# Optimization experiments

Hardware: AMD Instinct MI355X
Metric: run time of the kernel (lower is better)

The kernel has to match this reference:

```python
import jax, jax.numpy as jnp
import numpy as np

B, C, N, K, H = 8, 32, 4096, 32, 4  # batch, d_model, num_points, knn, heads
D = C // H
LN_EPS = 1e-5
ATT_EPS = 1e-6


def setup_inputs() -> dict:
    key = jax.random.key(0)
    ks = jax.random.split(key, 12)
    s = 0.05
    return {
        "search_feat": jax.random.normal(ks[0], (B, C, N), jnp.float32),
        "search_xyz": jax.random.normal(ks[1], (B, N, 3), jnp.float32),
        # pos MLP: Linear(3,32)+ReLU+Linear(32,32), weights stored [in,out]
        "w_pos1": jax.random.normal(ks[2], (3, 32), jnp.float32) * s,
        "b_pos1": jnp.zeros((32,), jnp.float32),
        "w_pos2": jax.random.normal(ks[3], (32, 32), jnp.float32) * s,
        "b_pos2": jnp.zeros((32,), jnp.float32),
        "w_q": jax.random.normal(ks[4], (C, C), jnp.float32) * s,
        "w_k": jax.random.normal(ks[5], (C, C), jnp.float32) * s,
        "w_v": jax.random.normal(ks[6], (C, C), jnp.float32) * s,
        "w_merge": jax.random.normal(ks[7], (C, C), jnp.float32) * s,
        "ln1_g": jnp.ones((C,), jnp.float32),
        "ln1_b": jnp.zeros((C,), jnp.float32),
        "w_mlp1": jax.random.normal(ks[8], (2 * C, 2 * C), jnp.float32) * s,
        "w_mlp2": jax.random.normal(ks[9], (2 * C, C), jnp.float32) * s,
        "ln2_g": jnp.ones((C,), jnp.float32),
        "ln2_b": jnp.zeros((C,), jnp.float32),
    }


def _layernorm(x, g, b):
    m = jnp.mean(x, axis=-1, keepdims=True)
    v = jnp.mean((x - m) ** 2, axis=-1, keepdims=True)
    return g * (x - m) * jax.lax.rsqrt(v + LN_EPS) + b


def _elu1(x):
    return jax.nn.elu(x) + 1.0


def reference(search_feat, search_xyz, w_pos1, b_pos1, w_pos2, b_pos2,
              w_q, w_k, w_v, w_merge, ln1_g, ln1_b, w_mlp1, w_mlp2,
              ln2_g, ln2_b):
    b, c, n = search_feat.shape
    h, d, k = H, C // H, K

    xt = jnp.transpose(search_feat, (0, 2, 1))  # [B,N,C]
    # knn in feature space: pd = -||xi||^2 + 2 xi.xj - ||xj||^2 (neg sq dist)
    xx = jnp.sum(xt * xt, axis=-1)  # [B,N]
    pd = 2.0 * jnp.einsum('bnc,bmc->bnm', xt, xt) - xx[:, :, None] - xx[:, None, :]
    idx = jax.lax.top_k(pd, k)[1]  # [B,N,K] nearest (incl. self)

    gather = jax.vmap(lambda f, i: f[i])  # per-batch gather
    fea_knn = gather(xt, idx)            # [B,N,K,C]
    xyz_knn = gather(search_xyz, idx)    # [B,N,K,3]

    def pos_mlp(z):
        return jax.nn.relu(z @ w_pos1 + b_pos1) @ w_pos2 + b_pos2

    q_in = xt + pos_mlp(search_xyz)      # [B,N,C]  (query, L=1)
    kv_in = fea_knn + pos_mlp(xyz_knn)   # [B,N,K,C]

    Q = (q_in @ w_q).reshape(b, n, h, d)          # [B,N,H,D]
    Ky = (kv_in @ w_k).reshape(b, n, k, h, d)     # [B,N,K,H,D]
    V = (kv_in @ w_v).reshape(b, n, k, h, d)

    Qf = _elu1(Q)
    Kf = _elu1(Ky)
    Vn = V / k  # v_length = K
    KV = jnp.einsum('bnkhd,bnkhv->bnhdv', Kf, Vn)
    Z = 1.0 / (jnp.einsum('bnhd,bnhd->bnh', Qf, Kf.sum(axis=2)) + ATT_EPS)
    msg = jnp.einsum('bnhd,bnhdv,bnh->bnhv', Qf, KV, Z) * k  # [B,N,H,D]

    msg = msg.reshape(b, n, c) @ w_merge
    msg = _layernorm(msg, ln1_g, ln1_b)
    msg = jnp.concatenate([xt, msg], axis=-1)          # [B,N,2C]
    msg = jax.nn.relu(msg @ w_mlp1) @ w_mlp2           # [B,N,C]
    msg = _layernorm(msg, ln2_g, ln2_b)
    return jnp.transpose(xt + msg, (0, 2, 1))          # [B,C,N]
```

## Files before the change

kernel.cpp:

```cpp
#include <hip/hip_runtime.h>
#include <math.h>

#define BB 8
#define CC 32
#define NN 4096
#define KNN 32
#define NP (BB*NN)

#define OFF_XT  0u
#define OFF_QF  1048576u
#define OFF_KV  2097152u
#define OFF_XX  4194304u
#define OFF_IDX 4227072u
#define OFF_XH  5275648u
#define OFF_XL  5799936u
#define OFF_MSG 5275648u

typedef _Float16 f16x8 __attribute__((ext_vector_type(8)));
typedef float f32x4 __attribute__((ext_vector_type(4)));
typedef float f32x16 __attribute__((ext_vector_type(16)));
#define MFMA16(A,B,C) __builtin_amdgcn_mfma_f32_16x16x32_f16(A,B,C,0,0,0)
#define MFMA32(A,B,C) __builtin_amdgcn_mfma_f32_32x32x16_f16(A,B,C,0,0,0)

__device__ __forceinline__ float elu1(float x) {
    return x > 0.f ? x + 1.f : expf(x);
}

__global__ __launch_bounds__(256) void k_transpose(const float* __restrict__ feat,
                                                   float* __restrict__ xt,
                                                   _Float16* __restrict__ Xh,
                                                   _Float16* __restrict__ Xl,
                                                   float* __restrict__ xx) {
    __shared__ float tile[32][65];
    int b = blockIdx.y;
    int n0 = blockIdx.x * 64;
    int t = threadIdx.x;
    int nn = t & 63, cr = t >> 6;
#pragma unroll
    for (int r = 0; r < 8; ++r) {
        int c = r * 4 + cr;
        tile[c][nn] = feat[((size_t)b * 32 + c) * NN + n0 + nn];
    }
    __syncthreads();
    int c2 = t & 31, nr = t >> 5;
#pragma unroll
    for (int r = 0; r < 8; ++r) {
        int nl = r * 8 + nr;
        size_t gi = ((size_t)b * NN + n0 + nl) * 32 + c2;
        float v = tile[c2][nl];
        xt[gi] = v;
        _Float16 hv = (_Float16)v;
        Xh[gi] = hv;
        Xl[gi] = (_Float16)(v - (float)hv);
    }
    if (t < 64) {
        float s = 0.f;
#pragma unroll
        for (int c = 0; c < 32; ++c) { float u = tile[c][t]; s += u * u; }
        xx[(size_t)b * NN + n0 + t] = s;
    }
}

__global__ __launch_bounds__(256, 2) void k_prep(
        const float* __restrict__ xt, const float* __restrict__ xyz,
        const float* __restrict__ w_pos1, const float* __restrict__ b_pos1,
        const float* __restrict__ w_pos2, const float* __restrict__ b_pos2,
        const float* __restrict__ w_q, const float* __restrict__ w_k,
        const float* __restrict__ w_v,
        float* __restrict__ Qf, float* __restrict__ KV) {
    __shared__ float sW2[1024], sWq[1024], sWk[1024], sWv[1024];
    int t = threadIdx.x;
    for (int i = t; i < 1024; i += 256) {
        sW2[i] = w_pos2[i];
        sWq[i] = w_q[i];
        sWk[i] = w_k[i];
        sWv[i] = w_v[i];
    }
    int lane = t & 31;
    int g = t >> 5;
    float w1c0 = w_pos1[lane], w1c1 = w_pos1[32 + lane], w1c2 = w_pos1[64 + lane];
    float b1c = b_pos1[lane], b2c = b_pos2[lane];
    __syncthreads();
#pragma unroll 1
    for (int p = blockIdx.x * 8 + g; p < NP; p += gridDim.x * 8) {
        asm volatile("" ::: "memory");
        float x0 = xyz[(size_t)p * 3 + 0];
        float x1 = xyz[(size_t)p * 3 + 1];
        float x2 = xyz[(size_t)p * 3 + 2];
        float h = fmaxf(x0 * w1c0 + x1 * w1c1 + x2 * w1c2 + b1c, 0.f);
        float P = b2c;
#pragma unroll 8
        for (int j = 0; j < 32; ++j) P += __shfl(h, j, 32) * sW2[j * 32 + lane];
        float xv = xt[(size_t)p * 32 + lane];
        float qin = xv + P;
        float qa = 0.f, ka = 0.f, va = 0.f;
#pragma unroll 8
        for (int j = 0; j < 32; ++j) {
            float qj = __shfl(qin, j, 32);
            qa += qj * sWq[j * 32 + lane];
            ka += qj * sWk[j * 32 + lane];
            va += qj * sWv[j * 32 + lane];
        }
        Qf[(size_t)p * 32 + lane] = elu1(qa);
        float2 kvv;
        kvv.x = elu1(ka);
        kvv.y = va;
        *(((float2*)(KV + (size_t)p * 64)) + lane) = kvv;
    }
}

__global__ __launch_bounds__(256, 2) void k_knn(
        const _Float16* __restrict__ Xh, const _Float16* __restrict__ Xl,
        const float* __restrict__ xt, const float* __restrict__ xx,
        unsigned* __restrict__ idxg) {
    __shared__ unsigned histU[32 * 132];
    __shared__ unsigned outIdx[32][32];
    __shared__ unsigned tieIdx[32][128];
    __shared__ int sT[32];
    __shared__ unsigned sBase[32];
    __shared__ unsigned outCnt[32], tieCnt[32];
    __shared__ float sM2;
    __shared__ float redbuf[4];

    int bid = blockIdx.x;
    int b = bid & 7;
    int n0 = (bid >> 3) << 5;
    int t = threadIdx.x;
    int lane = t & 63, wv = t >> 6;
    size_t bbase = (size_t)b * NN;

    for (int i = t; i < 32 * 132; i += 256) histU[i] = 0u;
    if (t < 32) { outCnt[t] = 0u; tieCnt[t] = 0u; }

    float lm = 0.f;
    for (int i = t; i < NN; i += 256) lm = fmaxf(lm, xx[bbase + i]);
#pragma unroll
    for (int off = 32; off >= 1; off >>= 1) lm = fmaxf(lm, __shfl_xor(lm, off, 64));
    if (lane == 0) redbuf[wv] = lm;
    __syncthreads();
    if (t == 0) sM2 = fmaxf(fmaxf(redbuf[0], redbuf[1]), fmaxf(redbuf[2], redbuf[3]));
    __syncthreads();
    float M = fmaxf(sM2, 1e-20f);

    const float C127 = 127.99f;
    float s = C127 / (4.f * M);
    float s2 = s + s;
    float sneg = -s;
    float o = 3.f * s * M;

    int cl31 = lane & 31;
    int hi = lane >> 5;
    int hi4 = hi << 2;
    const _Float16* Xhb = Xh + bbase * 32;
    const _Float16* Xlb = Xl + bbase * 32;
    const float* xxb = xx + bbase;

    const _Float16* ArH = Xhb + (size_t)(n0 + cl31) * 32;
    const _Float16* ArL = Xlb + (size_t)(n0 + cl31) * 32;
    f16x8 AhA = *(const f16x8*)(ArH + hi * 8);
    f16x8 AhB = *(const f16x8*)(ArH + 16 + hi * 8);
    f16x8 AlA = *(const f16x8*)(ArL + hi * 8);
    f16x8 AlB = *(const f16x8*)(ArL + 16 + hi * 8);

    unsigned colbase = (unsigned)(wv * 1024);
    unsigned hiB = (unsigned)hi * 16u;
    const char* XhbB = (const char*)Xhb;
    const char* XlbB = (const char*)Xlb;
    unsigned hi528 = (unsigned)hi * 528u;

    {
        unsigned cpc = colbase + cl31;
        f16x8 BhA_c = *(const f16x8*)(XhbB + cpc * 64u + hiB);
        f16x8 BhB_c = *(const f16x8*)(XhbB + cpc * 64u + hiB + 32u);
        f16x8 BlA_c = *(const f16x8*)(XlbB + cpc * 64u + hiB);
        f16x8 BlB_c = *(const f16x8*)(XlbB + cpc * 64u + hiB + 32u);
        float xxj_c = xxb[cpc];
#pragma unroll 1
        for (int tt = 0; tt < 32; ++tt) {
            unsigned cpn = colbase + (unsigned)(((tt + 1) & 31) << 5) + cl31;
            f16x8 BhA_n = *(const f16x8*)(XhbB + cpn * 64u + hiB);
            f16x8 BhB_n = *(const f16x8*)(XhbB + cpn * 64u + hiB + 32u);
            f16x8 BlA_n = *(const f16x8*)(XlbB + cpn * 64u + hiB);
            f16x8 BlB_n = *(const f16x8*)(XlbB + cpn * 64u + hiB + 32u);
            float xxj_n = xxb[cpn];
            f32x16 acc = {0.f};
            acc = MFMA32(AhA, BlA_c, acc); acc = MFMA32(AhB, BlB_c, acc);
            acc = MFMA32(AlA, BhA_c, acc); acc = MFMA32(AlB, BhB_c, acc);
            acc = MFMA32(AhA, BhA_c, acc); acc = MFMA32(AhB, BhB_c, acc);
            float e = __builtin_fmaf(sneg, xxj_c, o);
#pragma unroll
            for (int r = 0; r < 16; ++r) {
                float qv = __builtin_fmaf(acc[r], s2, e);
                float qc = fminf(qv, C127);
                unsigned bkt = (unsigned)qc;
                atomicAdd(&histU[(unsigned)(((r & 3) + 8 * (r >> 2)) * 132) + hi528 + bkt], 1u);
            }
            BhA_c = BhA_n; BhB_c = BhB_n; BlA_c = BlA_n; BlB_c = BlB_n; xxj_c = xxj_n;
        }
    }
    __syncthreads();

#pragma unroll 1
    for (int rr = 0; rr < 8; ++rr) {
        int row = wv * 8 + rr;
        const unsigned* Hr = histU + row * 132;
        unsigned cl = Hr[2 * lane], ch = Hr[2 * lane + 1];
        unsigned ss = cl + ch;
        unsigned acc = ss;
#pragma unroll
        for (int off = 1; off < 64; off <<= 1) {
            unsigned vv = __shfl_down(acc, off, 64);
            if (lane + off < 64) acc += vv;
        }
        unsigned run = acc - ss;
        int Tl = -1; unsigned bl = 0;
        if (run < 32u && run + ch >= 32u) { Tl = 2 * lane + 1; bl = run; }
        run += ch;
        if (Tl < 0 && run < 32u && run + cl >= 32u) { Tl = 2 * lane; bl = run; }
        unsigned long long bal = __ballot(Tl >= 0);
        int src = __ffsll(bal) - 1;
        int Tv = __shfl(Tl, src, 64);
        unsigned bv = (unsigned)__shfl((int)bl, src, 64);
        if (lane == 0) { sT[row] = Tv; sBase[row] = bv; }
    }
    __syncthreads();

    float Tlo16[16], Tin16[16];
#pragma unroll
    for (int r = 0; r < 16; ++r) {
        int rl = (r & 3) + 8 * (r >> 2) + hi4;
        int T = sT[rl];
        Tin16[r] = (float)(T + 1);
        Tlo16[r] = (T == 0) ? -3.0e38f : (float)T;
    }

    {
        unsigned cpc = colbase + cl31;
        f16x8 BhA_c = *(const f16x8*)(XhbB + cpc * 64u + hiB);
        f16x8 BhB_c = *(const f16x8*)(XhbB + cpc * 64u + hiB + 32u);
        f16x8 BlA_c = *(const f16x8*)(XlbB + cpc * 64u + hiB);
        f16x8 BlB_c = *(const f16x8*)(XlbB + cpc * 64u + hiB + 32u);
        float xxj_c = xxb[cpc];
#pragma unroll 1
        for (int tt = 0; tt < 32; ++tt) {
            unsigned cp = colbase + (unsigned)(tt << 5) + cl31;
            unsigned cpn = colbase + (unsigned)(((tt + 1) & 31) << 5) + cl31;
            f16x8 BhA_n = *(const f16x8*)(XhbB + cpn * 64u + hiB);
            f16x8 BhB_n = *(const f16x8*)(XhbB + cpn * 64u + hiB + 32u);
            f16x8 BlA_n = *(const f16x8*)(XlbB + cpn * 64u + hiB);
            f16x8 BlB_n = *(const f16x8*)(XlbB + cpn * 64u + hiB + 32u);
            float xxj_n = xxb[cpn];
            f32x16 acc = {0.f};
            acc = MFMA32(AhA, BlA_c, acc); acc = MFMA32(AhB, BlB_c, acc);
            acc = MFMA32(AlA, BhA_c, acc); acc = MFMA32(AlB, BhB_c, acc);
            acc = MFMA32(AhA, BhA_c, acc); acc = MFMA32(AhB, BhB_c, acc);
            float e = __builtin_fmaf(sneg, xxj_c, o);
#pragma unroll
            for (int r = 0; r < 16; ++r) {
                float qv = __builtin_fmaf(acc[r], s2, e);
                if (qv >= Tlo16[r]) {
                    unsigned rl = (unsigned)((r & 3) + 8 * (r >> 2) + hi4);
                    if (qv >= Tin16[r]) {
                        unsigned pos = atomicAdd(&outCnt[rl], 1u);
                        outIdx[rl][pos] = cp;
                    } else {
                        unsigned tp = atomicAdd(&tieCnt[rl], 1u);
                        if (tp < 128u) tieIdx[rl][tp] = cp;
                    }
                }
            }
            BhA_c = BhA_n; BhB_c = BhB_n; BlA_c = BlA_n; BlB_c = BlB_n; xxj_c = xxj_n;
        }
    }
    __syncthreads();

#pragma unroll 1
    for (int rr = 0; rr < 8; ++rr) {
        int row = wv * 8 + rr;
        int gr = n0 + row;
        unsigned bA = sBase[row];
        int need = 32 - (int)bA;
        if (need <= 0) continue;
        int nt = (int)tieCnt[row]; if (nt > 128) nt = 128;
        const float* xr = xt + (bbase + gr) * 32;
        float xxi_r = xxb[gr];
        float v0 = -INFINITY, v1 = -INFINITY;
        int i0 = 0x7fffffff, i1 = 0x7fffffff;
        bool a0v = lane < nt, a1v = lane + 64 < nt;
        if (a0v) {
            int c = (int)tieIdx[row][lane];
            const float* xc = xt + (bbase + c) * 32;
            float dot = 0.f;
#pragma unroll
            for (int ch = 0; ch < 32; ch += 4) {
                float4 rv = *(const float4*)(xr + ch);
                float4 cv = *(const float4*)(xc + ch);
                dot = __builtin_fmaf(rv.x, cv.x, dot);
                dot = __builtin_fmaf(rv.y, cv.y, dot);
                dot = __builtin_fmaf(rv.z, cv.z, dot);
                dot = __builtin_fmaf(rv.w, cv.w, dot);
            }
            v0 = 2.f * dot - xxi_r - xxb[c];
            i0 = c;
        }
        if (a1v) {
            int c = (int)tieIdx[row][lane + 64];
            const float* xc = xt + (bbase + c) * 32;
            float dot = 0.f;
#pragma unroll
            for (int ch = 0; ch < 32; ch += 4) {
                float4 rv = *(const float4*)(xr + ch);
                float4 cv = *(const float4*)(xc + ch);
                dot = __builtin_fmaf(rv.x, cv.x, dot);
                dot = __builtin_fmaf(rv.y, cv.y, dot);
                dot = __builtin_fmaf(rv.z, cv.z, dot);
                dot = __builtin_fmaf(rv.w, cv.w, dot);
            }
            v1 = 2.f * dot - xxi_r - xxb[c];
            i1 = c;
        }
        for (int it = 0; it < need; ++it) {
            float bvv = -INFINITY; int bj2 = 0x7fffffff;
            if (a0v && (v0 > bvv || (v0 == bvv && i0 < bj2))) { bvv = v0; bj2 = i0; }
            if (a1v && (v1 > bvv || (v1 == bvv && i1 < bj2))) { bvv = v1; bj2 = i1; }
#pragma unroll
            for (int off = 1; off < 64; off <<= 1) {
                float ov = __shfl_xor(bvv, off, 64);
                int oj = __shfl_xor(bj2, off, 64);
                if (ov > bvv || (ov == bvv && oj < bj2)) { bvv = ov; bj2 = oj; }
            }
            if (a0v && i0 == bj2) a0v = false;
            if (a1v && i1 == bj2) a1v = false;
            if (lane == 0) outIdx[row][bA + it] = (unsigned)bj2;
        }
    }
    __syncthreads();

    for (int i = t; i < 1024; i += 256)
        idxg[(bbase + n0 + (i >> 5)) * 32 + (i & 31)] = outIdx[i >> 5][i & 31];
}

__global__ __launch_bounds__(256) void k_attn(
        const float* __restrict__ Qf, const float* __restrict__ KV,
        const unsigned* __restrict__ idxg, float* __restrict__ msg) {
    int t = threadIdx.x;
    int wv = t >> 6, lane = t & 63;
    int l32 = lane & 31;
    int bid = blockIdx.x;
    int b = bid & 7;
    int p = b * NN + (bid >> 3) * 8 + wv * 2 + (lane >> 5);
    size_t bbase = (size_t)b * NN;
    const char* KVb = (const char*)(KV + bbase * 64);
    float q = Qf[(size_t)p * 32 + l32];
    int jv = (int)idxg[(size_t)p * 32 + l32];
    unsigned laneoff = (unsigned)l32 * 8u;
    float zacc = 0.f, macc = 0.f;
#pragma unroll 8
    for (int k = 0; k < 32; ++k) {
        int j = __shfl(jv, k, 32);
        unsigned off = ((unsigned)j << 8) + laneoff;
        float2 kv = *(const float2*)(KVb + off);
        float s = q * kv.x;
        s += __shfl_xor(s, 1, 8);
        s += __shfl_xor(s, 2, 8);
        s += __shfl_xor(s, 4, 8);
        zacc += s;
        macc = __builtin_fmaf(s, kv.y, macc);
    }
    float Z = 1.f / (zacc + 1e-6f);
    msg[(size_t)p * 32 + l32] = macc * Z;
}

__global__ __launch_bounds__(256, 2) void k_post(
        const float* __restrict__ msg, const float* __restrict__ xt,
        const float* __restrict__ w_merge,
        const float* __restrict__ ln1_g, const float* __restrict__ ln1_b,
        const float* __restrict__ w_mlp1, const float* __restrict__ w_mlp2,
        const float* __restrict__ ln2_g, const float* __restrict__ ln2_b,
        float* __restrict__ out) {
    __shared__ _Float16 wmT[2][32][32];
    __shared__ _Float16 w1T[2][64][64];
    __shared__ _Float16 w2T[2][32][64];
    __shared__ _Float16 sPh[4][16][40], sPl[4][16][40];
    __shared__ _Float16 sHh[4][16][72], sHl[4][16][72];
    int t = threadIdx.x;
    for (int i = t; i < 1024; i += 256) {
        float v = w_merge[i]; int in = i >> 5, o = i & 31;
        _Float16 h = (_Float16)v;
        wmT[0][o][in] = h; wmT[1][o][in] = (_Float16)(v - (float)h);
    }
    for (int i = t; i < 4096; i += 256) {
        float v = w_mlp1[i]; int in = i >> 6, o = i & 63;
        _Float16 h = (_Float16)v;
        w1T[0][o][in] = h; w1T[1][o][in] = (_Float16)(v - (float)h);
    }
    for (int i = t; i < 2048; i += 256) {
        float v = w_mlp2[i]; int in = i >> 5, o = i & 31;
        _Float16 h = (_Float16)v;
        w2T[0][o][in] = h; w2T[1][o][in] = (_Float16)(v - (float)h);
    }
    int wv = t >> 6, lane = t & 63;
    int row = lane & 15, kg = lane >> 4;
    int p0 = blockIdx.x * 64 + wv * 16;
    int b = p0 >> 12;
    float g1a = ln1_g[row], b1a = ln1_b[row], g1b = ln1_g[row + 16], b1b = ln1_b[row + 16];
    float g2a = ln2_g[row], b2a = ln2_b[row], g2b = ln2_g[row + 16], b2b = ln2_b[row + 16];
    __syncthreads();

    f32x4 z4 = {0.f, 0.f, 0.f, 0.f};
    f16x8 Amh, Aml;
    {
        const float* mr = msg + (size_t)(p0 + row) * 32 + kg * 8;
#pragma unroll
        for (int j = 0; j < 8; ++j) {
            float v = mr[j];
            _Float16 h = (_Float16)v;
            Amh[j] = h; Aml[j] = (_Float16)(v - (float)h);
        }
    }
    f32x4 accM[2];
#pragma unroll
    for (int n = 0; n < 2; ++n) {
        f16x8 Bh = *(const f16x8*)&wmT[0][n * 16 + row][kg * 8];
        f16x8 Bl = *(const f16x8*)&wmT[1][n * 16 + row][kg * 8];
        f32x4 a = z4;
        a = MFMA16(Aml, Bl, a); a = MFMA16(Amh, Bl, a);
        a = MFMA16(Aml, Bh, a); a = MFMA16(Amh, Bh, a);
        accM[n] = a;
    }
#pragma unroll
    for (int r = 0; r < 4; ++r) {
        float s0 = accM[0][r], s1 = accM[1][r];
        float sm = s0 + s1;
        sm += __shfl_xor(sm, 1, 64); sm += __shfl_xor(sm, 2, 64);
        sm += __shfl_xor(sm, 4, 64); sm += __shfl_xor(sm, 8, 64);
        float mean = sm * (1.f / 32.f);
        float d0 = s0 - mean, d1 = s1 - mean;
        float vv = d0 * d0 + d1 * d1;
        vv += __shfl_xor(vv, 1, 64); vv += __shfl_xor(vv, 2, 64);
        vv += __shfl_xor(vv, 4, 64); vv += __shfl_xor(vv, 8, 64);
        float rst = rsqrtf(vv * (1.f / 32.f) + 1e-5f);
        float m0 = g1a * d0 * rst + b1a;
        float m1 = g1b * d1 * rst + b1b;
        int pl = kg * 4 + r;
        _Float16 h0 = (_Float16)m0;
        sPh[wv][pl][row] = h0; sPl[wv][pl][row] = (_Float16)(m0 - (float)h0);
        _Float16 h1 = (_Float16)m1;
        sPh[wv][pl][row + 16] = h1; sPl[wv][pl][row + 16] = (_Float16)(m1 - (float)h1);
    }
    __syncthreads();
    f16x8 Axh, Axl;
    {
        const float* xr = xt + (size_t)(p0 + row) * 32 + kg * 8;
#pragma unroll
        for (int j = 0; j < 8; ++j) {
            float v = xr[j];
            _Float16 h = (_Float16)v;
            Axh[j] = h; Axl[j] = (_Float16)(v - (float)h);
        }
    }
    f16x8 Aph = *(const f16x8*)&sPh[wv][row][kg * 8];
    f16x8 Apl = *(const f16x8*)&sPl[wv][row][kg * 8];
    f32x4 accH[4];
#pragma unroll
    for (int n = 0; n < 4; ++n) {
        f16x8 B0h = *(const f16x8*)&w1T[0][n * 16 + row][kg * 8];
        f16x8 B0l = *(const f16x8*)&w1T[1][n * 16 + row][kg * 8];
        f16x8 B1h = *(const f16x8*)&w1T[0][n * 16 + row][32 + kg * 8];
        f16x8 B1l = *(const f16x8*)&w1T[1][n * 16 + row][32 + kg * 8];
        f32x4 a = z4;
        a = MFMA16(Axl, B0l, a); a = MFMA16(Axh, B0l, a);
        a = MFMA16(Axl, B0h, a); a = MFMA16(Axh, B0h, a);
        a = MFMA16(Apl, B1l, a); a = MFMA16(Aph, B1l, a);
        a = MFMA16(Apl, B1h, a); a = MFMA16(Aph, B1h, a);
        accH[n] = a;
    }
#pragma unroll
    for (int n = 0; n < 4; ++n) {
#pragma unroll
        for (int r = 0; r < 4; ++r) {
            float hv = fmaxf(accH[n][r], 0.f);
            int pl = kg * 4 + r;
            _Float16 hh = (_Float16)hv;
            sHh[wv][pl][n * 16 + row] = hh;
            sHl[wv][pl][n * 16 + row] = (_Float16)(hv - (float)hh);
        }
    }
    __syncthreads();
    f16x8 Hh0 = *(const f16x8*)&sHh[wv][row][kg * 8];
    f16x8 Hl0 = *(const f16x8*)&sHl[wv][row][kg * 8];
    f16x8 Hh1 = *(const f16x8*)&sHh[wv][row][32 + kg * 8];
    f16x8 Hl1 = *(const f16x8*)&sHl[wv][row][32 + kg * 8];
    f32x4 accO[2];
#pragma unroll
    for (int n = 0; n < 2; ++n) {
        f16x8 B0h = *(const f16x8*)&w2T[0][n * 16 + row][kg * 8];
        f16x8 B0l = *(const f16x8*)&w2T[1][n * 16 + row][kg * 8];
        f16x8 B1h = *(const f16x8*)&w2T[0][n * 16 + row][32 + kg * 8];
        f16x8 B1l = *(const f16x8*)&w2T[1][n * 16 + row][32 + kg * 8];
        f32x4 a = z4;
        a = MFMA16(Hl0, B0l, a); a = MFMA16(Hh0, B0l, a);
        a = MFMA16(Hl0, B0h, a); a = MFMA16(Hh0, B0h, a);
        a = MFMA16(Hl1, B1l, a); a = MFMA16(Hh1, B1l, a);
        a = MFMA16(Hl1, B1h, a); a = MFMA16(Hh1, B1h, a);
        accO[n] = a;
    }
#pragma unroll
    for (int r = 0; r < 4; ++r) {
        float s0 = accO[0][r], s1 = accO[1][r];
        float sm = s0 + s1;
        sm += __shfl_xor(sm, 1, 64); sm += __shfl_xor(sm, 2, 64);
        sm += __shfl_xor(sm, 4, 64); sm += __shfl_xor(sm, 8, 64);
        float mean = sm * (1.f / 32.f);
        float d0 = s0 - mean, d1 = s1 - mean;
        float vv = d0 * d0 + d1 * d1;
        vv += __shfl_xor(vv, 1, 64); vv += __shfl_xor(vv, 2, 64);
        vv += __shfl_xor(vv, 4, 64); vv += __shfl_xor(vv, 8, 64);
        float rst = rsqrtf(vv * (1.f / 32.f) + 1e-5f);
        float o0 = g2a * d0 * rst + b2a;
        float o1 = g2b * d1 * rst + b2b;
        int pt = p0 + kg * 4 + r;
        int nb = pt & 4095;
        float xv0 = xt[(size_t)pt * 32 + row];
        float xv1 = xt[(size_t)pt * 32 + row + 16];
        out[((size_t)b * 32 + row) * 4096 + nb] = xv0 + o0;
        out[((size_t)b * 32 + row + 16) * 4096 + nb] = xv1 + o1;
    }
}

extern "C" void kernel_launch(void* const* d_in, const int* in_sizes, int n_in,
                              void* d_out, int out_size, void* d_ws, size_t ws_size,
                              hipStream_t stream) {
    const float* feat   = (const float*)d_in[0];
    const float* xyz    = (const float*)d_in[1];
    const float* w_pos1 = (const float*)d_in[2];
    const float* b_pos1 = (const float*)d_in[3];
    const float* w_pos2 = (const float*)d_in[4];
    const float* b_pos2 = (const float*)d_in[5];
    const float* w_q    = (const float*)d_in[6];
    const float* w_k    = (const float*)d_in[7];
    const float* w_v    = (const float*)d_in[8];
    const float* w_mg   = (const float*)d_in[9];
    const float* ln1_g  = (const float*)d_in[10];
    const float* ln1_b  = (const float*)d_in[11];
    const float* w_mlp1 = (const float*)d_in[12];
    const float* w_mlp2 = (const float*)d_in[13];
    const float* ln2_g  = (const float*)d_in[14];
    const float* ln2_b  = (const float*)d_in[15];
    float* ws = (float*)d_ws;
    float* xt = ws + OFF_XT;
    float* Qf = ws + OFF_QF;
    float* KVp = ws + OFF_KV;
    float* xx = ws + OFF_XX;
    unsigned* idxg = (unsigned*)(ws + OFF_IDX);
    _Float16* Xh = (_Float16*)(ws + OFF_XH);
    _Float16* Xl = (_Float16*)(ws + OFF_XL);
    float* msg = ws + OFF_MSG;
    float* out = (float*)d_out;

    k_transpose<<<dim3(64, 8), 256, 0, stream>>>(feat, xt, Xh, Xl, xx);
    k_prep<<<1024, 256, 0, stream>>>(xt, xyz, w_pos1, b_pos1, w_pos2, b_pos2,
                                     w_q, w_k, w_v, Qf, KVp);
    k_knn<<<1024, 256, 0, stream>>>(Xh, Xl, xt, xx, idxg);
    k_attn<<<4096, 256, 0, stream>>>(Qf, KVp, idxg, msg);
    k_post<<<512, 256, 0, stream>>>(msg, xt, w_mg, ln1_g, ln1_b,
                                    w_mlp1, w_mlp2, ln2_g, ln2_b, out);
}
```

Baseline: 271.1 us.

## Prune kNN histogram atomics with an early threshold floor and split MFMA chains

The histogram pass now runs in two phases. A first sample of column tiles builds a provisional histogram, from which a per-row floor bucket is derived. The remaining tiles then only add histogram atomics for scores at or above that floor, which cuts most of the LDS atomic traffic. The emit pass compares integer buckets instead of float thresholds. The MFMA accumulation is split into two independent chains, and the loops are manually double-buffered with alternating register sets. The floor logic adds complexity and relies on the sampled tiles giving a valid lower bound for each row's top-32.

After: 357.7 us. 31.9% more time.

```diff
diff --git a/kernel.cpp b/kernel.cpp
--- a/kernel.cpp
+++ b/kernel.cpp
@@ -109,6 +109,54 @@
     }
 }
 
+#define LOADB(S, ttv) \
+    { unsigned cp_ = colbase + ((unsigned)(ttv) << 5) + cl31; \
+      S##hA = *(const f16x8*)(XhbB + cp_ * 64u + hiB); \
+      S##hB = *(const f16x8*)(XhbB + cp_ * 64u + hiB + 32u); \
+      S##lA = *(const f16x8*)(XlbB + cp_ * 64u + hiB); \
+      S##lB = *(const f16x8*)(XlbB + cp_ * 64u + hiB + 32u); \
+      S##xx = xxb[cp_]; }
+
+#define SCORES(S) \
+      f32x16 aX = {0.f}, aY = {0.f}; \
+      aX = MFMA32(AhA, S##lA, aX); aY = MFMA32(AhB, S##lB, aY); \
+      aX = MFMA32(AlA, S##hA, aX); aY = MFMA32(AlB, S##hB, aY); \
+      aX = MFMA32(AhA, S##hA, aX); aY = MFMA32(AhB, S##hB, aY); \
+      float e = __builtin_fmaf(sneg, S##xx, o);
+
+#define ROWC(r) (((r) & 3) + 8 * ((r) >> 2))
+
+#define EP_HISTA(S) { SCORES(S) \
+      _Pragma("unroll") \
+      for (int r = 0; r < 16; ++r) { \
+        float qv = __builtin_fmaf(aX[r], s2, __builtin_fmaf(aY[r], s2, e)); \
+        float qc = __builtin_amdgcn_fmed3f(qv, 0.f, C127); \
+        atomicAdd(&histU[(unsigned)(ROWC(r) * 132) + hi528 + (unsigned)qc], 1u); } }
+
+#define EP_HISTB(S) { SCORES(S) \
+      _Pragma("unroll") \
+      for (int r = 0; r < 16; ++r) { \
+        float qv = __builtin_fmaf(aX[r], s2, __builtin_fmaf(aY[r], s2, e)); \
+        if (qv >= fb16[r]) { \
+          float qc = __builtin_amdgcn_fmed3f(qv, 0.f, C127); \
+          atomicAdd(&histU[(unsigned)(ROWC(r) * 132) + hi528 + (unsigned)qc], 1u); } } }
+
+#define EP_EMIT(S, ttv) { SCORES(S) \
+      unsigned cpE = colbase + ((unsigned)(ttv) << 5) + cl31; \
+      _Pragma("unroll") \
+      for (int r = 0; r < 16; ++r) { \
+        float qv = __builtin_fmaf(aX[r], s2, __builtin_fmaf(aY[r], s2, e)); \
+        float qc = __builtin_amdgcn_fmed3f(qv, 0.f, C127); \
+        int bkt = (int)(unsigned)qc; \
+        if (bkt >= Ti16[r]) { \
+          unsigned rl = (unsigned)(ROWC(r) + hi4); \
+          if (bkt > Ti16[r]) { \
+            unsigned pos = atomicAdd(&outCnt[rl], 1u); \
+            outIdx[rl][pos] = cpE; \
+          } else { \
+            unsigned tp = atomicAdd(&tieCnt[rl], 1u); \
+            if (tp < 128u) tieIdx[rl][tp] = cpE; } } } }
+
 __global__ __launch_bounds__(256, 2) void k_knn(
         const _Float16* __restrict__ Xh, const _Float16* __restrict__ Xl,
         const float* __restrict__ xt, const float* __restrict__ xx,
@@ -118,6 +166,7 @@
     __shared__ unsigned tieIdx[32][128];
     __shared__ int sT[32];
     __shared__ unsigned sBase[32];
+    __shared__ float sFloor[32];
     __shared__ unsigned outCnt[32], tieCnt[32];
     __shared__ float sM2;
     __shared__ float redbuf[4];
@@ -166,37 +215,55 @@
     unsigned hiB = (unsigned)hi * 16u;
     const char* XhbB = (const char*)Xhb;
     const char* XlbB = (const char*)Xlb;
-    unsigned hi528 = (unsigned)hi * 528u;
-
-    {
-        unsigned cpc = colbase + cl31;
-        f16x8 BhA_c = *(const f16x8*)(XhbB + cpc * 64u + hiB);
-        f16x8 BhB_c = *(const f16x8*)(XhbB + cpc * 64u + hiB + 32u);
-        f16x8 BlA_c = *(const f16x8*)(XlbB + cpc * 64u + hiB);
-        f16x8 BlB_c = *(const f16x8*)(XlbB + cpc * 64u + hiB + 32u);
-        float xxj_c = xxb[cpc];
+    unsigned hi528 = (unsigned)hi4 * 132u;
+
+    f16x8 PhA, PhB, PlA, PlB; float Pxx;
+    f16x8 QhA, QhB, QlA, QlB; float Qxx;
+
+    LOADB(P, 0)
 #pragma unroll 1
-        for (int tt = 0; tt < 32; ++tt) {
-            unsigned cpn = colbase + (unsigned)(((tt + 1) & 31) << 5) + cl31;
-            f16x8 BhA_n = *(const f16x8*)(XhbB + cpn * 64u + hiB);
-            f16x8 BhB_n = *(const f16x8*)(XhbB + cpn * 64u + hiB + 32u);
-            f16x8 BlA_n = *(const f16x8*)(XlbB + cpn * 64u + hiB);
-            f16x8 BlB_n = *(const f16x8*)(XlbB + cpn * 64u + hiB + 32u);
-            float xxj_n = xxb[cpn];
-            f32x16 acc = {0.f};
-            acc = MFMA32(AhA, BlA_c, acc); acc = MFMA32(AhB, BlB_c, acc);
-            acc = MFMA32(AlA, BhA_c, acc); acc = MFMA32(AlB, BhB_c, acc);
-            acc = MFMA32(AhA, BhA_c, acc); acc = MFMA32(AhB, BhB_c, acc);
-            float e = __builtin_fmaf(sneg, xxj_c, o);
-#pragma unroll
-            for (int r = 0; r < 16; ++r) {
-                float qv = __builtin_fmaf(acc[r], s2, e);
-                float qc = fminf(qv, C127);
-                unsigned bkt = (unsigned)qc;
-                atomicAdd(&histU[(unsigned)(((r & 3) + 8 * (r >> 2)) * 132) + hi528 + bkt], 1u);
-            }
-            BhA_c = BhA_n; BhB_c = BhB_n; BlA_c = BlA_n; BlB_c = BlB_n; xxj_c = xxj_n;
-        }
+    for (int tt = 0; tt < 4; tt += 2) {
+        LOADB(Q, tt + 1)
+        EP_HISTA(P)
+        LOADB(P, tt + 2)
+        EP_HISTA(Q)
+    }
+    __syncthreads();
+
+#pragma unroll 1
+    for (int rr = 0; rr < 8; ++rr) {
+        int row = wv * 8 + rr;
+        const unsigned* Hr = histU + row * 132;
+        unsigned cl = Hr[2 * lane], ch = Hr[2 * lane + 1];
+        unsigned ss = cl + ch;
+        unsigned acc = ss;
+#pragma unroll
+        for (int off = 1; off < 64; off <<= 1) {
+            unsigned vv = __shfl_down(acc, off, 64);
+            if (lane + off < 64) acc += vv;
+        }
+        unsigned run = acc - ss;
+        int Tl = -1;
+        if (run < 32u && run + ch >= 32u) Tl = 2 * lane + 1;
+        run += ch;
+        if (Tl < 0 && run < 32u && run + cl >= 32u) Tl = 2 * lane;
+        unsigned long long bal = __ballot(Tl >= 0);
+        int src = __ffsll(bal) - 1;
+        int Tv = __shfl(Tl, src, 64);
+        if (lane == 0) sFloor[row] = (Tv <= 0) ? -3.0e38f : (float)Tv;
+    }
+    __syncthreads();
+
+    float fb16[16];
+#pragma unroll
+    for (int r = 0; r < 16; ++r) fb16[r] = sFloor[ROWC(r) + hi4];
+
+#pragma unroll 1
+    for (int tt = 4; tt < 32; tt += 2) {
+        LOADB(Q, tt + 1)
+        EP_HISTB(P)
+        LOADB(P, (tt + 2 < 32) ? (tt + 2) : 0)
+        EP_HISTB(Q)
     }
     __syncthreads();
 
@@ -225,52 +292,16 @@
     }
     __syncthreads();
 
-    float Tlo16[16], Tin16[16];
-#pragma unroll
-    for (int r = 0; r < 16; ++r) {
-        int rl = (r & 3) + 8 * (r >> 2) + hi4;
-        int T = sT[rl];
-        Tin16[r] = (float)(T + 1);
-        Tlo16[r] = (T == 0) ? -3.0e38f : (float)T;
-    }
-
-    {
-        unsigned cpc = colbase + cl31;
-        f16x8 BhA_c = *(const f16x8*)(XhbB + cpc * 64u + hiB);
-        f16x8 BhB_c = *(const f16x8*)(XhbB + cpc * 64u + hiB + 32u);
-        f16x8 BlA_c = *(const f16x8*)(XlbB + cpc * 64u + hiB);
-        f16x8 BlB_c = *(const f16x8*)(XlbB + cpc * 64u + hiB + 32u);
-        float xxj_c = xxb[cpc];
+    int Ti16[16];
+#pragma unroll
+    for (int r = 0; r < 16; ++r) Ti16[r] = sT[ROWC(r) + hi4];
+
 #pragma unroll 1
-        for (int tt = 0; tt < 32; ++tt) {
-            unsigned cp = colbase + (unsigned)(tt << 5) + cl31;
-            unsigned cpn = colbase + (unsigned)(((tt + 1) & 31) << 5) + cl31;
-            f16x8 BhA_n = *(const f16x8*)(XhbB + cpn * 64u + hiB);
-            f16x8 BhB_n = *(const f16x8*)(XhbB + cpn * 64u + hiB + 32u);
-            f16x8 BlA_n = *(const f16x8*)(XlbB + cpn * 64u + hiB);
-            f16x8 BlB_n = *(const f16x8*)(XlbB + cpn * 64u + hiB + 32u);
-            float xxj_n = xxb[cpn];
-            f32x16 acc = {0.f};
-            acc = MFMA32(AhA, BlA_c, acc); acc = MFMA32(AhB, BlB_c, acc);
-            acc = MFMA32(AlA, BhA_c, acc); acc = MFMA32(AlB, BhB_c, acc);
-            acc = MFMA32(AhA, BhA_c, acc); acc = MFMA32(AhB, BhB_c, acc);
-            float e = __builtin_fmaf(sneg, xxj_c, o);
-#pragma unroll
-            for (int r = 0; r < 16; ++r) {
-                float qv = __builtin_fmaf(acc[r], s2, e);
-                if (qv >= Tlo16[r]) {
-                    unsigned rl = (unsigned)((r & 3) + 8 * (r >> 2) + hi4);
-                    if (qv >= Tin16[r]) {
-                        unsigned pos = atomicAdd(&outCnt[rl], 1u);
-                        outIdx[rl][pos] = cp;
-                    } else {
-                        unsigned tp = atomicAdd(&tieCnt[rl], 1u);
-                        if (tp < 128u) tieIdx[rl][tp] = cp;
-                    }
-                }
-            }
-            BhA_c = BhA_n; BhB_c = BhB_n; BlA_c = BlA_n; BlB_c = BlB_n; xxj_c = xxj_n;
-        }
+    for (int tt = 0; tt < 32; tt += 2) {
+        LOADB(Q, tt + 1)
+        EP_EMIT(P, tt)
+        LOADB(P, (tt + 2 < 32) ? (tt + 2) : 0)
+        EP_EMIT(Q, tt + 1)
     }
     __syncthreads();
 
@@ -339,6 +370,13 @@
     for (int i = t; i < 1024; i += 256)
         idxg[(bbase + n0 + (i >> 5)) * 32 + (i & 31)] = outIdx[i >> 5][i & 31];
 }
+
+#undef LOADB
+#undef SCORES
+#undef ROWC
+#undef EP_HISTA
+#undef EP_HISTB
+#undef EP_EMIT
 
 __global__ __launch_bounds__(256) void k_attn(
         const float* __restrict__ Qf, const float* __restrict__ KV,
```
